# Kernel optimization log

Measured on AMD Instinct MI355X. Metric: run time of the kernel, lower is better.

## Reference

```python
import jax, jax.numpy as jnp
import numpy as np

N = 4096
SPECIES = 100
FEA = 64        # atom_emb_dim
NBR_FEA = 64    # num gaussians
MAX_NBRS = 12
LN_EPS = 1e-5

# GaussianSmearing constants: linspace(0, 8, 64)
_OFFSET = jnp.linspace(0.0, 8.0, NBR_FEA)
_COEFF = -0.5 / float(8.0 / (NBR_FEA - 1)) ** 2


def _uniform(key, shape, fan_in):
    s = 1.0 / np.sqrt(fan_in)
    return jax.random.uniform(key, shape, minval=-s, maxval=s, dtype=jnp.float32)


def setup_inputs() -> dict:
    key = jax.random.key(0)
    ks = jax.random.split(key, 20)
    lat_pred = jnp.eye(3, dtype=jnp.float32) * 8.0 + 0.2 * jax.random.normal(ks[0], (3, 3), dtype=jnp.float32)
    fracs_pred = jax.random.uniform(ks[1], (N, 3), dtype=jnp.float32)
    species_logits = jax.random.normal(ks[2], (N, SPECIES), dtype=jnp.float32)
    occ_logits = jax.random.normal(ks[3], (N,), dtype=jnp.float32)
    # params
    emb_w = _uniform(ks[4], (SPECIES, FEA), SPECIES)
    emb_b = _uniform(ks[5], (FEA,), SPECIES)
    in1 = 2 * FEA + NBR_FEA  # 192
    w1 = _uniform(ks[6], (in1, 2 * FEA), in1)
    b1 = _uniform(ks[7], (2 * FEA,), in1)
    g1 = jnp.ones((2 * FEA,), jnp.float32)
    be1 = jnp.zeros((2 * FEA,), jnp.float32)
    w2 = _uniform(ks[8], (in1, 2 * FEA), in1)
    b2 = _uniform(ks[9], (2 * FEA,), in1)
    g2 = jnp.ones((2 * FEA,), jnp.float32)
    be2 = jnp.zeros((2 * FEA,), jnp.float32)
    fc_w = _uniform(ks[10], (FEA, 1), FEA)
    fc_b = _uniform(ks[11], (1,), FEA)
    return dict(lat_pred=lat_pred, fracs_pred=fracs_pred, species_logits=species_logits,
                occ_logits=occ_logits, emb_w=emb_w, emb_b=emb_b,
                w1=w1, b1=b1, g1=g1, be1=be1, w2=w2, b2=b2, g2=g2, be2=be2,
                fc_w=fc_w, fc_b=fc_b)


def _layernorm(x, g, b):
    m = jnp.mean(x, axis=-1, keepdims=True)
    v = jnp.var(x, axis=-1, keepdims=True)
    return (x - m) * jax.lax.rsqrt(v + LN_EPS) * g + b


def _cgcnn_layer(atom, nbr_atom, nbr_fea, w, b, g, be):
    # atom: [N,F]; nbr_atom: [N,M,F]; nbr_fea: [N,M,K]
    n, m = nbr_atom.shape[:2]
    atom_exp = jnp.broadcast_to(atom[:, None, :], (n, m, atom.shape[-1]))
    total = jnp.concatenate([atom_exp, nbr_atom, nbr_fea], axis=2)  # [N,M,2F+K]
    z = _layernorm(total @ w + b, g, be)                            # [N,M,2F]
    nbr_filter, nbr_core = jnp.split(z, 2, axis=2)
    nbr_sumed = jnp.sum(jax.nn.sigmoid(nbr_filter) * jax.nn.softplus(nbr_core), axis=1)
    return jax.nn.softplus(atom + nbr_sumed)


def reference(lat_pred, fracs_pred, species_logits, occ_logits,
              emb_w, emb_b, w1, b1, g1, be1, w2, b2, g2, be2, fc_w, fc_b):
    species_probs = jax.nn.softmax(species_logits, axis=-1)
    atom_fea = species_probs @ emb_w + emb_b                         # [N,F]
    diff = fracs_pred[:, None, :] - fracs_pred[None, :, :]           # [N,N,3]
    diff = diff - jnp.round(diff)                                    # min-image
    cart = diff @ lat_pred                                           # [N,N,3]
    dist = jnp.linalg.norm(cart, axis=-1)                            # [N,N]
    dist = dist + jnp.eye(dist.shape[0], dtype=dist.dtype) * 100.0
    k = min(MAX_NBRS, dist.shape[1] - 1)
    neg_d, nbr_idx = jax.lax.top_k(-dist, k)                         # smallest k
    nbr_dist = -neg_d                                                # [N,k]
    nbr_fea = jnp.exp(_COEFF * (nbr_dist[..., None] - _OFFSET) ** 2) # [N,k,K]
    nbr_atom_fea = atom_fea[nbr_idx]                                 # [N,k,F]
    atom_fea = _cgcnn_layer(atom_fea, nbr_atom_fea, nbr_fea, w1, b1, g1, be1)
    atom_fea = _cgcnn_layer(atom_fea, nbr_atom_fea, nbr_fea, w2, b2, g2, be2)
    occ_probs = jax.nn.sigmoid(occ_logits)[:, None]                  # [N,1]
    graph_fea = jnp.sum(atom_fea * occ_probs, axis=0) / (jnp.sum(occ_probs) + 1e-6)
    return graph_fea @ fc_w + fc_b                                   # [1]
```

## Files before the change

kernel.cpp:

```cpp
#include <hip/hip_runtime.h>
#include <math.h>

#define N_ATOMS 4096
#define SPECIES 100
#define FEA 64
#define M_NBR 12

typedef unsigned short u16;
typedef __attribute__((ext_vector_type(8))) _Float16 f16x8;
typedef __attribute__((ext_vector_type(4))) float f32x4;

constexpr float LN_EPS = 1e-5f;
constexpr float GAUSS_COEFF = -31.0078125f;
constexpr float D2_INF = 3.4e38f;

__device__ __forceinline__ float sigmoidf_(float x){
    return __fdividef(1.0f, 1.0f + __expf(-x));
}
__device__ __forceinline__ float softplusf_(float x){
    return fmaxf(x, 0.0f) + __logf(1.0f + __expf(-fabsf(x)));
}
__device__ __forceinline__ u16 f16bits(_Float16 h){ return *(u16*)&h; }

__global__ __launch_bounds__(256) void k_setup(const float* __restrict__ fracs,
        const float* __restrict__ w1, const float* __restrict__ w2,
        const float* __restrict__ logits, const float* __restrict__ emb_w,
        const float* __restrict__ emb_b,
        float* __restrict__ fx, float* __restrict__ fy, float* __restrict__ fz,
        u16* __restrict__ wpk, float* __restrict__ atom0, u16* __restrict__ a0f){
    __shared__ float sE[4][SPECIES];
    int b = blockIdx.x, t = threadIdx.x;
    if (b < 192){
        int gid = b * 256 + t;
        int layer = gid / 24576;
        int e = gid % 24576;
        int k = e >> 7, n = e & 127;
        float x = (layer ? w2 : w1)[e];
        int mat = layer * 3 + (k >> 6);
        int kk = k & 63;
        int ch = kk >> 5, lg2 = (kk >> 3) & 3, i = kk & 7;
        int nt = n >> 4, lr2 = n & 15;
        wpk[mat * 8192 + ((ch * 8 + nt) * 64 + (lg2 * 16 + lr2)) * 8 + i] = f16bits((_Float16)x);
    } else if (b < 208){
        int j = (b - 192) * 256 + t;
        fx[j] = fracs[j*3+0];
        fy[j] = fracs[j*3+1];
        fz[j] = fracs[j*3+2];
    } else {
        int grp = t >> 6, f = t & 63;
        int a = (b - 208) * 4 + grp;
        const float* lg = logits + (long)a * SPECIES;
        float l0 = lg[f];
        float l1 = (f + 64 < SPECIES) ? lg[f + 64] : -1e30f;
        float mx = fmaxf(l0, l1);
        #pragma unroll
        for (int off = 32; off; off >>= 1) mx = fmaxf(mx, __shfl_xor(mx, off));
        float e0 = __expf(l0 - mx);
        float e1 = (f + 64 < SPECIES) ? __expf(l1 - mx) : 0.0f;
        sE[grp][f] = e0;
        if (f + 64 < SPECIES) sE[grp][64 + f] = e1;
        float sm = e0 + e1;
        #pragma unroll
        for (int off = 32; off; off >>= 1) sm += __shfl_xor(sm, off);
        __syncthreads();
        float acc = 0.0f;
        for (int s = 0; s < SPECIES; ++s) acc += sE[grp][s] * emb_w[s * FEA + f];
        float v = acc / sm + emb_b[f];
        atom0[(long)a * FEA + f] = v;
        a0f[a * FEA + f] = f16bits((_Float16)v);
    }
}

__global__ __launch_bounds__(256) void k_topk(const float* __restrict__ fx,
        const float* __restrict__ fy, const float* __restrict__ fz,
        const float* __restrict__ lat, int* __restrict__ nbr_idx,
        float* __restrict__ nbr_dist){
    __shared__ int   hist[256];
    __shared__ int   cnt;
    __shared__ float sThr;
    __shared__ float candD[256];
    __shared__ int   candI[256];
    int i = blockIdx.x, tid = threadIdx.x;
    hist[tid] = 0;
    if (tid == 0) cnt = 0;
    __syncthreads();
    float l00=lat[0],l01=lat[1],l02=lat[2];
    float l10=lat[3],l11=lat[4],l12=lat[5];
    float l20=lat[6],l21=lat[7],l22=lat[8];
    float xi = fx[i], yi = fy[i], zi = fz[i];
    float d2r[16];
    #pragma unroll
    for (int k = 0; k < 16; ++k){
        int j = tid + k * 256;
        float dx = xi - fx[j];
        float dy = yi - fy[j];
        float dz = zi - fz[j];
        dx -= rintf(dx); dy -= rintf(dy); dz -= rintf(dz);
        float cx = dx*l00 + dy*l10 + dz*l20;
        float cy = dx*l01 + dy*l11 + dz*l21;
        float cz = dx*l02 + dy*l12 + dz*l22;
        float d2 = cx*cx + cy*cy + cz*cz;
        if (j == i) d2 = D2_INF;
        d2r[k] = d2;
        if (d2 < 4.0f) atomicAdd(&hist[(int)(d2 * 64.0f)], 1);
    }
    __syncthreads();
    if (tid < 64){
        int s0 = hist[4*tid] + hist[4*tid+1] + hist[4*tid+2] + hist[4*tid+3];
        int sc = s0;
        #pragma unroll
        for (int off = 1; off < 64; off <<= 1){
            int o = __shfl_up(sc, off);
            if (tid >= off) sc += o;
        }
        unsigned long long mball = __ballot(sc >= M_NBR);
        if (mball == 0ULL){
            if (tid == 0) sThr = 1e30f;
        } else {
            int gbin = __ffsll(mball) - 1;
            if (tid == gbin){
                int c = sc - s0;
                float th = 4.0f;
                #pragma unroll
                for (int b = 0; b < 4; ++b){
                    c += hist[4*gbin + b];
                    if (c >= M_NBR){ th = (float)(4*gbin + b + 1) * (1.0f/64.0f); break; }
                }
                sThr = th;
            }
        }
    }
    __syncthreads();
    float thr = sThr;
    #pragma unroll
    for (int k = 0; k < 16; ++k){
        if (d2r[k] < thr){
            int p = atomicAdd(&cnt, 1);
            if (p < 256){ candD[p] = d2r[k]; candI[p] = tid + k * 256; }
        }
    }
    __syncthreads();
    int n = cnt < 256 ? cnt : 256;
    for (int c = tid; c < n; c += 256){
        float dv = candD[c]; int iv = candI[c];
        int rank = 0;
        for (int s = 0; s < n; ++s){
            float ds_ = candD[s]; int is_ = candI[s];
            rank += (ds_ < dv || (ds_ == dv && is_ < iv)) ? 1 : 0;
        }
        if (rank < M_NBR){
            nbr_idx[i * M_NBR + rank]  = iv;
            nbr_dist[i * M_NBR + rank] = sqrtf(dv);
        }
    }
}

__global__ __launch_bounds__(192) void k_fused(
        const float* __restrict__ atom0F, const u16* __restrict__ a0f,
        const int* __restrict__ nbr_idx, const float* __restrict__ nbr_dist,
        const u16* __restrict__ wpk,
        const float* __restrict__ b1, const float* __restrict__ g1, const float* __restrict__ be1,
        const float* __restrict__ b2, const float* __restrict__ g2, const float* __restrict__ be2,
        float* __restrict__ outF)
{
    __shared__ u16   wlds[24576];
    __shared__ float prod[96][65];
    __shared__ float sSF[8][64];
    __shared__ u16   sSH[8][64];
    __shared__ float sS[8][132];

    const int t = threadIdx.x;
    const int w = t >> 6, l = t & 63;
    const int lg = l >> 4, lr = l & 15;
    const int blk = blockIdx.x;

    {
        const float4* wsrc = (const float4*)wpk;
        float4* wdst = (float4*)wlds;
        #pragma unroll
        for (int it = 0; it < 16; ++it)
            wdst[it * 192 + t] = wsrc[it * 192 + t];
    }

    int nid[2]; float dist[2];
    #pragma unroll
    for (int mt = 0; mt < 2; ++mt){
        int row = blk * 96 + w * 32 + mt * 16 + lr;
        nid[mt]  = nbr_idx[row];
        dist[mt] = nbr_dist[row];
    }
    f16x8 nfr[2][2];
    #pragma unroll
    for (int mt = 0; mt < 2; ++mt){
        nfr[mt][0] = *(const f16x8*)(a0f + nid[mt] * 64 + lg * 8);
        nfr[mt][1] = *(const f16x8*)(a0f + nid[mt] * 64 + 32 + lg * 8);
    }
    f16x8 saf[2];
    #pragma unroll
    for (int c = 0; c < 2; ++c)
        saf[c] = (w == 0 && lr < 8) ? *(const f16x8*)(a0f + (blk * 8 + lr) * 64 + c * 32 + lg * 8)
                                    : (f16x8)0;
    float res[3];
    res[0] = atom0F[(long)blk * 512 + t];
    res[1] = atom0F[(long)blk * 512 + 192 + t];
    res[2] = (t < 128) ? atom0F[(long)blk * 512 + 384 + t] : 0.0f;

    float g1v[8], be1v[8], g2v[8], be2v[8], b1v[8], b2v[8];
    #pragma unroll
    for (int nt = 0; nt < 8; ++nt){
        int c = nt * 16 + lr;
        g1v[nt] = g1[c]; be1v[nt] = be1[c];
        g2v[nt] = g2[c]; be2v[nt] = be2[c];
        b1v[nt] = b1[c]; b2v[nt] = b2[c];
    }

    f16x8 ga[2][2];
    #pragma unroll
    for (int mt = 0; mt < 2; ++mt)
        #pragma unroll
        for (int c = 0; c < 2; ++c)
            #pragma unroll
            for (int i = 0; i < 8; ++i){
                int k = c * 32 + lg * 8 + i;
                float dd = dist[mt] - (float)k * (8.0f / 63.0f);
                ga[mt][c][i] = (_Float16)__expf(GAUSS_COEFF * dd * dd);
            }

    int aloc[2][4];
    #pragma unroll
    for (int mt = 0; mt < 2; ++mt)
        #pragma unroll
        for (int rr = 0; rr < 4; ++rr)
            aloc[mt][rr] = (w * 32 + mt * 16 + lg * 4 + rr) / 12;

    const u16* wlS = wlds;
    const u16* wlN = wlds + 8192;
    const u16* wlG = wlds + 16384;

    __syncthreads();

    if (w == 0){
        f32x4 a1[8];
        #pragma unroll
        for (int nt = 0; nt < 8; ++nt) a1[nt] = 0.0f;
        #pragma unroll
        for (int c = 0; c < 2; ++c)
            #pragma unroll
            for (int nt = 0; nt < 8; ++nt){
                const f16x8 b = *(const f16x8*)(wlS + ((c * 8 + nt) * 64 + l) * 8);
                a1[nt] = __builtin_amdgcn_mfma_f32_16x16x32_f16(saf[c], b, a1[nt], 0, 0, 0);
            }
        if (lg < 2){
            #pragma unroll
            for (int nt = 0; nt < 8; ++nt)
                #pragma unroll
                for (int rr = 0; rr < 4; ++rr)
                    sS[lg * 4 + rr][nt * 16 + lr] = a1[nt][rr] + b1v[nt];
        }
    }
    f32x4 acc[2][8];
    #pragma unroll
    for (int mt = 0; mt < 2; ++mt)
        #pragma unroll
        for (int nt = 0; nt < 8; ++nt) acc[mt][nt] = 0.0f;
    #pragma unroll
    for (int c = 0; c < 2; ++c)
        #pragma unroll
        for (int nt = 0; nt < 8; ++nt){
            const f16x8 bn = *(const f16x8*)(wlN + ((c * 8 + nt) * 64 + l) * 8);
            const f16x8 bg = *(const f16x8*)(wlG + ((c * 8 + nt) * 64 + l) * 8);
            #pragma unroll
            for (int mt = 0; mt < 2; ++mt){
                acc[mt][nt] = __builtin_amdgcn_mfma_f32_16x16x32_f16(nfr[mt][c], bn, acc[mt][nt], 0, 0, 0);
                acc[mt][nt] = __builtin_amdgcn_mfma_f32_16x16x32_f16(ga[mt][c],  bg, acc[mt][nt], 0, 0, 0);
            }
        }
    __syncthreads();

    #pragma unroll
    for (int mt = 0; mt < 2; ++mt){
        float s[4] = {0,0,0,0}, q[4] = {0,0,0,0};
        #pragma unroll
        for (int nt = 0; nt < 8; ++nt)
            #pragma unroll
            for (int rr = 0; rr < 4; ++rr){
                float v = acc[mt][nt][rr] + sS[aloc[mt][rr]][nt * 16 + lr];
                acc[mt][nt][rr] = v;
                s[rr] += v; q[rr] += v * v;
            }
        #pragma unroll
        for (int rr = 0; rr < 4; ++rr){
            #pragma unroll
            for (int m = 1; m < 16; m <<= 1){
                s[rr] += __shfl_xor(s[rr], m);
                q[rr] += __shfl_xor(q[rr], m);
            }
        }
        #pragma unroll
        for (int rr = 0; rr < 4; ++rr){
            float mean = s[rr] * (1.0f / 128.0f);
            float var  = q[rr] * (1.0f / 128.0f) - mean * mean;
            float inv  = rsqrtf(var + LN_EPS);
            #pragma unroll
            for (int nt = 0; nt < 4; ++nt){
                float zf = (acc[mt][nt][rr]     - mean) * inv * g1v[nt]     + be1v[nt];
                float zc = (acc[mt][nt + 4][rr] - mean) * inv * g1v[nt + 4] + be1v[nt + 4];
                prod[w * 32 + mt * 16 + lg * 4 + rr][nt * 16 + lr] = sigmoidf_(zf) * softplusf_(zc);
            }
        }
    }
    {
        const float4* wsrc2 = (const float4*)(wpk + 3 * 8192);
        float4* wdst = (float4*)wlds;
        #pragma unroll
        for (int it = 0; it < 16; ++it)
            wdst[it * 192 + t] = wsrc2[it * 192 + t];
    }
    __syncthreads();

    {
        int a_ = t >> 6, c = t & 63;
        float sm = 0.0f;
        #pragma unroll
        for (int m = 0; m < 12; ++m) sm += prod[a_ * 12 + m][c];
        float o = softplusf_(res[0] + sm);
        sSF[a_][c] = o; sSH[a_][c] = f16bits((_Float16)o);

        int i2 = t + 192; int a2_ = i2 >> 6, c2 = i2 & 63;
        float sm2 = 0.0f;
        #pragma unroll
        for (int m = 0; m < 12; ++m) sm2 += prod[a2_ * 12 + m][c2];
        float o2 = softplusf_(res[1] + sm2);
        sSF[a2_][c2] = o2; sSH[a2_][c2] = f16bits((_Float16)o2);

        if (t < 128){
            int i3 = t + 384; int a3_ = i3 >> 6, c3 = i3 & 63;
            float sm3 = 0.0f;
            #pragma unroll
            for (int m = 0; m < 12; ++m) sm3 += prod[a3_ * 12 + m][c3];
            float o3 = softplusf_(res[2] + sm3);
            sSF[a3_][c3] = o3; sSH[a3_][c3] = f16bits((_Float16)o3);
        }
    }
    __syncthreads();

    if (w == 1){
        f16x8 af[2];
        #pragma unroll
        for (int c = 0; c < 2; ++c)
            af[c] = (lr < 8) ? *(const f16x8*)(&sSH[lr][c * 32 + lg * 8]) : (f16x8)0;
        f32x4 a2[8];
        #pragma unroll
        for (int nt = 0; nt < 8; ++nt) a2[nt] = 0.0f;
        #pragma unroll
        for (int c = 0; c < 2; ++c)
            #pragma unroll
            for (int nt = 0; nt < 8; ++nt){
                const f16x8 b = *(const f16x8*)(wlS + ((c * 8 + nt) * 64 + l) * 8);
                a2[nt] = __builtin_amdgcn_mfma_f32_16x16x32_f16(af[c], b, a2[nt], 0, 0, 0);
            }
        if (lg < 2){
            #pragma unroll
            for (int nt = 0; nt < 8; ++nt)
                #pragma unroll
                for (int rr = 0; rr < 4; ++rr)
                    sS[lg * 4 + rr][nt * 16 + lr] = a2[nt][rr] + b2v[nt];
        }
    }
    f32x4 acc2[2][8];
    #pragma unroll
    for (int mt = 0; mt < 2; ++mt)
        #pragma unroll
        for (int nt = 0; nt < 8; ++nt) acc2[mt][nt] = 0.0f;
    #pragma unroll
    for (int c = 0; c < 2; ++c)
        #pragma unroll
        for (int nt = 0; nt < 8; ++nt){
            const f16x8 bn = *(const f16x8*)(wlN + ((c * 8 + nt) * 64 + l) * 8);
            const f16x8 bg = *(const f16x8*)(wlG + ((c * 8 + nt) * 64 + l) * 8);
            #pragma unroll
            for (int mt = 0; mt < 2; ++mt){
                acc2[mt][nt] = __builtin_amdgcn_mfma_f32_16x16x32_f16(nfr[mt][c], bn, acc2[mt][nt], 0, 0, 0);
                acc2[mt][nt] = __builtin_amdgcn_mfma_f32_16x16x32_f16(ga[mt][c],  bg, acc2[mt][nt], 0, 0, 0);
            }
        }
    __syncthreads();

    #pragma unroll
    for (int mt = 0; mt < 2; ++mt){
        float s[4] = {0,0,0,0}, q[4] = {0,0,0,0};
        #pragma unroll
        for (int nt = 0; nt < 8; ++nt)
            #pragma unroll
            for (int rr = 0; rr < 4; ++rr){
                float v = acc2[mt][nt][rr] + sS[aloc[mt][rr]][nt * 16 + lr];
                acc2[mt][nt][rr] = v;
                s[rr] += v; q[rr] += v * v;
            }
        #pragma unroll
        for (int rr = 0; rr < 4; ++rr){
            #pragma unroll
            for (int m = 1; m < 16; m <<= 1){
                s[rr] += __shfl_xor(s[rr], m);
                q[rr] += __shfl_xor(q[rr], m);
            }
        }
        #pragma unroll
        for (int rr = 0; rr < 4; ++rr){
            float mean = s[rr] * (1.0f / 128.0f);
            float var  = q[rr] * (1.0f / 128.0f) - mean * mean;
            float inv  = rsqrtf(var + LN_EPS);
            #pragma unroll
            for (int nt = 0; nt < 4; ++nt){
                float zf = (acc2[mt][nt][rr]     - mean) * inv * g2v[nt]     + be2v[nt];
                float zc = (acc2[mt][nt + 4][rr] - mean) * inv * g2v[nt + 4] + be2v[nt + 4];
                prod[w * 32 + mt * 16 + lg * 4 + rr][nt * 16 + lr] = sigmoidf_(zf) * softplusf_(zc);
            }
        }
    }
    __syncthreads();

    {
        int a_ = t >> 6, c = t & 63;
        float sm = 0.0f;
        #pragma unroll
        for (int m = 0; m < 12; ++m) sm += prod[a_ * 12 + m][c];
        outF[(long)blk * 512 + t] = softplusf_(sSF[a_][c] + sm);

        int i2 = t + 192; int a2_ = i2 >> 6, c2 = i2 & 63;
        float sm2 = 0.0f;
        #pragma unroll
        for (int m = 0; m < 12; ++m) sm2 += prod[a2_ * 12 + m][c2];
        outF[(long)blk * 512 + i2] = softplusf_(sSF[a2_][c2] + sm2);

        if (t < 128){
            int i3 = t + 384; int a3_ = i3 >> 6, c3 = i3 & 63;
            float sm3 = 0.0f;
            #pragma unroll
            for (int m = 0; m < 12; ++m) sm3 += prod[a3_ * 12 + m][c3];
            outF[(long)blk * 512 + i3] = softplusf_(sSF[a3_][c3] + sm3);
        }
    }
}

__global__ __launch_bounds__(256) void k_partial(const float* __restrict__ atom,
        const float* __restrict__ occ, float* __restrict__ partials){
    int b = blockIdx.x, tid = threadIdx.x;
    int f = tid & 63, sub = tid >> 6;
    __shared__ float sAcc[256];
    float acc = 0.0f;
    for (int it = 0; it < 16; ++it){
        int a = b * 64 + sub + it * 4;
        float p = sigmoidf_(occ[a]);
        acc += atom[(long)a * FEA + f] * p;
    }
    sAcc[tid] = acc;
    __syncthreads();
    if (tid < 64){
        float s = sAcc[f] + sAcc[64 + f] + sAcc[128 + f] + sAcc[192 + f];
        partials[b * 65 + f] = s;
        float po = sigmoidf_(occ[b * 64 + f]);
        #pragma unroll
        for (int off = 32; off; off >>= 1) po += __shfl_down(po, off);
        if (f == 0) partials[b * 65 + 64] = po;
    }
}

__global__ __launch_bounds__(64) void k_final(const float* __restrict__ partials,
        const float* __restrict__ fc_w, const float* __restrict__ fc_b,
        float* __restrict__ out){
    int f = threadIdx.x;
    float num = 0.0f;
    for (int p = 0; p < 64; ++p) num += partials[p * 65 + f];
    float occs = partials[f * 65 + 64];
    #pragma unroll
    for (int off = 32; off; off >>= 1) occs += __shfl_down(occs, off);
    occs = __shfl(occs, 0);
    float gf = num / (occs + 1e-6f);
    float v = gf * fc_w[f];
    #pragma unroll
    for (int off = 32; off; off >>= 1) v += __shfl_down(v, off);
    if (f == 0) out[0] = v + fc_b[0];
}

extern "C" void kernel_launch(void* const* d_in, const int* in_sizes, int n_in,
                              void* d_out, int out_size, void* d_ws, size_t ws_size,
                              hipStream_t stream) {
    const float* lat    = (const float*)d_in[0];
    const float* fracs  = (const float*)d_in[1];
    const float* slog   = (const float*)d_in[2];
    const float* occ    = (const float*)d_in[3];
    const float* emb_w  = (const float*)d_in[4];
    const float* emb_b  = (const float*)d_in[5];
    const float* w1     = (const float*)d_in[6];
    const float* b1     = (const float*)d_in[7];
    const float* g1     = (const float*)d_in[8];
    const float* be1    = (const float*)d_in[9];
    const float* w2     = (const float*)d_in[10];
    const float* b2     = (const float*)d_in[11];
    const float* g2     = (const float*)d_in[12];
    const float* be2    = (const float*)d_in[13];
    const float* fc_w   = (const float*)d_in[14];
    const float* fc_b   = (const float*)d_in[15];
    float* out = (float*)d_out;

    char* ws = (char*)d_ws;
    auto alloc = [&](size_t bytes) -> void* {
        void* p = (void*)ws;
        ws += (bytes + 255) & ~(size_t)255;
        return p;
    };
    int*   nbr_idx  = (int*)  alloc((size_t)N_ATOMS * M_NBR * 4);
    float* nbr_dist = (float*)alloc((size_t)N_ATOMS * M_NBR * 4);
    float* atom0    = (float*)alloc((size_t)N_ATOMS * FEA * 4);
    float* atom1    = (float*)alloc((size_t)N_ATOMS * FEA * 4);
    u16*   a0f      = (u16*)  alloc((size_t)N_ATOMS * FEA * 2);
    u16*   wpk      = (u16*)  alloc((size_t)6 * 8192 * 2);
    float* fxa      = (float*)alloc((size_t)N_ATOMS * 4);
    float* fya      = (float*)alloc((size_t)N_ATOMS * 4);
    float* fza      = (float*)alloc((size_t)N_ATOMS * 4);
    float* partials = (float*)alloc((size_t)64 * 65 * 4);

    k_setup  <<<208 + N_ATOMS / 4, 256, 0, stream>>>(fracs, w1, w2, slog, emb_w, emb_b,
                fxa, fya, fza, wpk, atom0, a0f);
    k_topk   <<<N_ATOMS, 256, 0, stream>>>(fxa, fya, fza, lat, nbr_idx, nbr_dist);
    k_fused  <<<N_ATOMS / 8, 192, 0, stream>>>(atom0, a0f, nbr_idx, nbr_dist,
                wpk, b1, g1, be1, b2, g2, be2, atom1);
    k_partial<<<64, 256, 0, stream>>>(atom1, occ, partials);
    k_final  <<<1, 64, 0, stream>>>(partials, fc_w, fc_b, out);
}
```

Before: 63.58 us.

## Read MFMA weights directly from global memory and drop LDS weight staging

Removes the cooperative copy of packed weights into LDS (two 48KB stages) and has each wave load its B fragments straight from global memory, which the cache should serve. Each wave now computes the self-atom projection redundantly into its own sSw slice, which removes two block barriers. LDS use drops sharply, which may raise occupancy, at the cost of redundant self-projection MFMAs and global/L2 latency on the weight fragments. The g2/be2/b2 loads are also deferred to cut register pressure.

```diff
diff --git a/kernel.cpp b/kernel.cpp
--- a/kernel.cpp
+++ b/kernel.cpp
@@ -163,25 +163,16 @@
         const float* __restrict__ b2, const float* __restrict__ g2, const float* __restrict__ be2,
         float* __restrict__ outF)
 {
-    __shared__ u16   wlds[24576];
+    __shared__ float sSw[3][8][132];
     __shared__ float prod[96][65];
     __shared__ float sSF[8][64];
     __shared__ u16   sSH[8][64];
-    __shared__ float sS[8][132];
 
     const int t = threadIdx.x;
     const int w = t >> 6, l = t & 63;
     const int lg = l >> 4, lr = l & 15;
     const int blk = blockIdx.x;
 
-    {
-        const float4* wsrc = (const float4*)wpk;
-        float4* wdst = (float4*)wlds;
-        #pragma unroll
-        for (int it = 0; it < 16; ++it)
-            wdst[it * 192 + t] = wsrc[it * 192 + t];
-    }
-
     int nid[2]; float dist[2];
     #pragma unroll
     for (int mt = 0; mt < 2; ++mt){
@@ -198,20 +189,18 @@
     f16x8 saf[2];
     #pragma unroll
     for (int c = 0; c < 2; ++c)
-        saf[c] = (w == 0 && lr < 8) ? *(const f16x8*)(a0f + (blk * 8 + lr) * 64 + c * 32 + lg * 8)
-                                    : (f16x8)0;
+        saf[c] = (lr < 8) ? *(const f16x8*)(a0f + (blk * 8 + lr) * 64 + c * 32 + lg * 8)
+                          : (f16x8)0;
     float res[3];
     res[0] = atom0F[(long)blk * 512 + t];
     res[1] = atom0F[(long)blk * 512 + 192 + t];
     res[2] = (t < 128) ? atom0F[(long)blk * 512 + 384 + t] : 0.0f;
 
-    float g1v[8], be1v[8], g2v[8], be2v[8], b1v[8], b2v[8];
+    float g1v[8], be1v[8], b1v[8];
     #pragma unroll
     for (int nt = 0; nt < 8; ++nt){
         int c = nt * 16 + lr;
-        g1v[nt] = g1[c]; be1v[nt] = be1[c];
-        g2v[nt] = g2[c]; be2v[nt] = be2[c];
-        b1v[nt] = b1[c]; b2v[nt] = b2[c];
+        g1v[nt] = g1[c]; be1v[nt] = be1[c]; b1v[nt] = b1[c];
     }
 
     f16x8 ga[2][2];
@@ -233,13 +222,14 @@
         for (int rr = 0; rr < 4; ++rr)
             aloc[mt][rr] = (w * 32 + mt * 16 + lg * 4 + rr) / 12;
 
-    const u16* wlS = wlds;
-    const u16* wlN = wlds + 8192;
-    const u16* wlG = wlds + 16384;
-
-    __syncthreads();
-
-    if (w == 0){
+    const u16* ws1 = wpk;
+    const u16* wn1 = wpk + 1 * 8192;
+    const u16* wg1 = wpk + 2 * 8192;
+    const u16* ws2 = wpk + 3 * 8192;
+    const u16* wn2 = wpk + 4 * 8192;
+    const u16* wg2 = wpk + 5 * 8192;
+
+    {
         f32x4 a1[8];
         #pragma unroll
         for (int nt = 0; nt < 8; ++nt) a1[nt] = 0.0f;
@@ -247,7 +237,7 @@
         for (int c = 0; c < 2; ++c)
             #pragma unroll
             for (int nt = 0; nt < 8; ++nt){
-                const f16x8 b = *(const f16x8*)(wlS + ((c * 8 + nt) * 64 + l) * 8);
+                const f16x8 b = *(const f16x8*)(ws1 + ((c * 8 + nt) * 64 + l) * 8);
                 a1[nt] = __builtin_amdgcn_mfma_f32_16x16x32_f16(saf[c], b, a1[nt], 0, 0, 0);
             }
         if (lg < 2){
@@ -255,9 +245,10 @@
             for (int nt = 0; nt < 8; ++nt)
                 #pragma unroll
                 for (int rr = 0; rr < 4; ++rr)
-                    sS[lg * 4 + rr][nt * 16 + lr] = a1[nt][rr] + b1v[nt];
-        }
-    }
+                    sSw[w][lg * 4 + rr][nt * 16 + lr] = a1[nt][rr] + b1v[nt];
+        }
+    }
+
     f32x4 acc[2][8];
     #pragma unroll
     for (int mt = 0; mt < 2; ++mt)
@@ -267,15 +258,14 @@
     for (int c = 0; c < 2; ++c)
         #pragma unroll
         for (int nt = 0; nt < 8; ++nt){
-            const f16x8 bn = *(const f16x8*)(wlN + ((c * 8 + nt) * 64 + l) * 8);
-            const f16x8 bg = *(const f16x8*)(wlG + ((c * 8 + nt) * 64 + l) * 8);
+            const f16x8 bn = *(const f16x8*)(wn1 + ((c * 8 + nt) * 64 + l) * 8);
+            const f16x8 bg = *(const f16x8*)(wg1 + ((c * 8 + nt) * 64 + l) * 8);
             #pragma unroll
             for (int mt = 0; mt < 2; ++mt){
                 acc[mt][nt] = __builtin_amdgcn_mfma_f32_16x16x32_f16(nfr[mt][c], bn, acc[mt][nt], 0, 0, 0);
                 acc[mt][nt] = __builtin_amdgcn_mfma_f32_16x16x32_f16(ga[mt][c],  bg, acc[mt][nt], 0, 0, 0);
             }
         }
-    __syncthreads();
 
     #pragma unroll
     for (int mt = 0; mt < 2; ++mt){
@@ -284,7 +274,7 @@
         for (int nt = 0; nt < 8; ++nt)
             #pragma unroll
             for (int rr = 0; rr < 4; ++rr){
-                float v = acc[mt][nt][rr] + sS[aloc[mt][rr]][nt * 16 + lr];
+                float v = acc[mt][nt][rr] + sSw[w][aloc[mt][rr]][nt * 16 + lr];
                 acc[mt][nt][rr] = v;
                 s[rr] += v; q[rr] += v * v;
             }
@@ -309,13 +299,6 @@
             }
         }
     }
-    {
-        const float4* wsrc2 = (const float4*)(wpk + 3 * 8192);
-        float4* wdst = (float4*)wlds;
-        #pragma unroll
-        for (int it = 0; it < 16; ++it)
-            wdst[it * 192 + t] = wsrc2[it * 192 + t];
-    }
     __syncthreads();
 
     {
@@ -344,11 +327,18 @@
     }
     __syncthreads();
 
-    if (w == 1){
-        f16x8 af[2];
+    float g2v[8], be2v[8], b2v[8];
+    #pragma unroll
+    for (int nt = 0; nt < 8; ++nt){
+        int c = nt * 16 + lr;
+        g2v[nt] = g2[c]; be2v[nt] = be2[c]; b2v[nt] = b2[c];
+    }
+
+    {
+        f16x8 af2[2];
         #pragma unroll
         for (int c = 0; c < 2; ++c)
-            af[c] = (lr < 8) ? *(const f16x8*)(&sSH[lr][c * 32 + lg * 8]) : (f16x8)0;
+            af2[c] = (lr < 8) ? *(const f16x8*)(&sSH[lr][c * 32 + lg * 8]) : (f16x8)0;
         f32x4 a2[8];
         #pragma unroll
         for (int nt = 0; nt < 8; ++nt) a2[nt] = 0.0f;
@@ -356,17 +346,18 @@
         for (int c = 0; c < 2; ++c)
             #pragma unroll
             for (int nt = 0; nt < 8; ++nt){
-                const f16x8 b = *(const f16x8*)(wlS + ((c * 8 + nt) * 64 + l) * 8);
-                a2[nt] = __builtin_amdgcn_mfma_f32_16x16x32_f16(af[c], b, a2[nt], 0, 0, 0);
+                const f16x8 b = *(const f16x8*)(ws2 + ((c * 8 + nt) * 64 + l) * 8);
+                a2[nt] = __builtin_amdgcn_mfma_f32_16x16x32_f16(af2[c], b, a2[nt], 0, 0, 0);
             }
         if (lg < 2){
             #pragma unroll
             for (int nt = 0; nt < 8; ++nt)
                 #pragma unroll
                 for (int rr = 0; rr < 4; ++rr)
-                    sS[lg * 4 + rr][nt * 16 + lr] = a2[nt][rr] + b2v[nt];
-        }
-    }
+                    sSw[w][lg * 4 + rr][nt * 16 + lr] = a2[nt][rr] + b2v[nt];
+        }
+    }
+
     f32x4 acc2[2][8];
     #pragma unroll
     for (int mt = 0; mt < 2; ++mt)
@@ -376,15 +367,14 @@
     for (int c = 0; c < 2; ++c)
         #pragma unroll
         for (int nt = 0; nt < 8; ++nt){
-            const f16x8 bn = *(const f16x8*)(wlN + ((c * 8 + nt) * 64 + l) * 8);
-            const f16x8 bg = *(const f16x8*)(wlG + ((c * 8 + nt) * 64 + l) * 8);
+            const f16x8 bn = *(const f16x8*)(wn2 + ((c * 8 + nt) * 64 + l) * 8);
+            const f16x8 bg = *(const f16x8*)(wg2 + ((c * 8 + nt) * 64 + l) * 8);
             #pragma unroll
             for (int mt = 0; mt < 2; ++mt){
                 acc2[mt][nt] = __builtin_amdgcn_mfma_f32_16x16x32_f16(nfr[mt][c], bn, acc2[mt][nt], 0, 0, 0);
                 acc2[mt][nt] = __builtin_amdgcn_mfma_f32_16x16x32_f16(ga[mt][c],  bg, acc2[mt][nt], 0, 0, 0);
             }
         }
-    __syncthreads();
 
     #pragma unroll
     for (int mt = 0; mt < 2; ++mt){
@@ -393,7 +383,7 @@
         for (int nt = 0; nt < 8; ++nt)
             #pragma unroll
             for (int rr = 0; rr < 4; ++rr){
-                float v = acc2[mt][nt][rr] + sS[aloc[mt][rr]][nt * 16 + lr];
+                float v = acc2[mt][nt][rr] + sSw[w][aloc[mt][rr]][nt * 16 + lr];
                 acc2[mt][nt][rr] = v;
                 s[rr] += v; q[rr] += v * v;
             }
```

Result: faster. 60.64 us (-4.6%).
